# Kernel tuning notes

Hardware: AMD Instinct MI355X
Metric: run time of the kernel (lower is better)

Reference implementation:

```python
import jax, jax.numpy as jnp
import numpy as np

DIM = 64
OUT_DIM = 32
ALPHA = 16
BRANCH = 4
DEPTH = 7  # levels 0..DEPTH; level l has BRANCH**l nodes
SIZES = [BRANCH ** l for l in range(DEPTH + 1)]
OFFS = np.cumsum([0] + SIZES).tolist()  # OFFS[l] = start index of level l (BFS order)
N = OFFS[-1]  # 21845


def _build_children():
    # complete 4-ary tree in BFS order; leaves get 0 (never read)
    ch = np.zeros((N, BRANCH), dtype=np.int32)
    for l in range(DEPTH):
        off, size = OFFS[l], SIZES[l]
        base = OFFS[l + 1] + BRANCH * np.arange(size)
        ch[off:off + size] = base[:, None] + np.arange(BRANCH)[None, :]
    return jnp.asarray(ch)


def setup_inputs() -> dict:
    key = jax.random.key(0)
    k1, k2, k3, k4, k5 = jax.random.split(key, 5)
    sym = jax.random.randint(k1, (N,), 0, ALPHA, dtype=jnp.int32)
    children = _build_children()
    s = 1.0 / np.sqrt(DIM)
    W = jax.random.normal(k2, (ALPHA, DIM, DIM), dtype=jnp.float32) * s      # per-symbol Linear weight [out,in]
    b = jax.random.normal(k3, (ALPHA, DIM), dtype=jnp.float32) * s           # per-symbol Linear bias
    W_out = jax.random.normal(k4, (OUT_DIM, DIM), dtype=jnp.float32) * s
    b_out = jax.random.normal(k5, (OUT_DIM,), dtype=jnp.float32) * s
    return {"sym": sym, "children": children, "W": W, "b": b,
            "W_out": W_out, "b_out": b_out}


def _forward(W, b, W_out, b_out, sym, children):
    enc = jnp.zeros((N, DIM), dtype=W.dtype)
    # process levels bottom-up (children before parents) -- batches the
    # original node-by-node stack recursion by tree depth
    for l in range(DEPTH, -1, -1):
        off, size = OFFS[l], SIZES[l]
        syms = sym[off:off + size]                      # [size]
        if l == DEPTH:
            # leaves: layer applied to zero vector
            h = jnp.zeros((size, DIM), dtype=W.dtype)
        else:
            ch = children[off:off + size]               # [size, 4]
            h = enc[ch].mean(axis=1)                    # gather children encodings + mean
        Wn = W[syms]                                    # [size, dim, dim] symbol-routed weights
        bn = b[syms]                                    # [size, dim]
        e = jax.nn.sigmoid(jnp.einsum('nij,nj->ni', Wn, h) + bn)
        enc = enc.at[off:off + size].set(e)
    # root is node 0 in BFS order
    return enc[0] @ W_out.T + b_out                     # [OUT_DIM]


def reference(sym, children, W, b, W_out, b_out):
    return _forward(W, b, W_out, b_out, sym, children)
```

## Files before the change

### kernel.cpp

```cpp
#include <hip/hip_runtime.h>

#define DIM 64


__device__ __forceinline__ float sigmoidf_(float x) {
    return 1.0f / (1.0f + __expf(-x));
}

__device__ __forceinline__ float matvec_sig(const float* __restrict__ W,
                                            const float* __restrict__ B,
                                            int s, int lane,
                                            const float* h) {
    const float4* wrow = reinterpret_cast<const float4*>(W + (size_t)s * DIM * DIM + lane * DIM);
    const float4* h4   = reinterpret_cast<const float4*>(h);
    float acc = B[s * DIM + lane];
#pragma unroll
    for (int j = 0; j < DIM / 4; ++j) {
        float4 wv = wrow[j];
        float4 hv = h4[j];
        acc = fmaf(wv.x, hv.x, acc);
        acc = fmaf(wv.y, hv.y, acc);
        acc = fmaf(wv.z, hv.z, acc);
        acc = fmaf(wv.w, hv.w, acc);
    }
    return sigmoidf_(acc);
}

__global__ __launch_bounds__(1024) void k_lvl654(const int* __restrict__ sym,
                                                 const float* __restrict__ W,
                                                 const float* __restrict__ B,
                                                 float* __restrict__ enc4) {
    __shared__ __align__(16) float h6[16][DIM];
    __shared__ __align__(16) float e6[16][DIM];
    __shared__ __align__(16) float h5[4][DIM];
    __shared__ __align__(16) float e5[4][DIM];
    __shared__ __align__(16) float h4s[DIM];

    const int tid  = threadIdx.x;
    const int lane = tid & 63;
    const int w    = tid >> 6;
    const int b    = blockIdx.x;

    {
        int leaf0 = 5461 + b * 64 + w * 4;
        float acc = 0.0f;
#pragma unroll
        for (int c = 0; c < 4; ++c) {
            acc += sigmoidf_(B[sym[leaf0 + c] * DIM + lane]);
        }
        h6[w][lane] = 0.25f * acc;
    }
    __syncthreads();
    e6[w][lane] = matvec_sig(W, B, sym[1365 + b * 16 + w], lane, &h6[w][0]);
    __syncthreads();
    if (w < 4) {
        h5[w][lane] = 0.25f * (e6[4 * w + 0][lane] + e6[4 * w + 1][lane] +
                               e6[4 * w + 2][lane] + e6[4 * w + 3][lane]);
    }
    __syncthreads();
    if (w < 4) {
        e5[w][lane] = matvec_sig(W, B, sym[341 + b * 4 + w], lane, &h5[w][0]);
    }
    __syncthreads();
    if (w == 0) {
        h4s[lane] = 0.25f * (e5[0][lane] + e5[1][lane] + e5[2][lane] + e5[3][lane]);
    }
    __syncthreads();
    if (w == 0) {
        enc4[b * DIM + lane] = matvec_sig(W, B, sym[85 + b], lane, h4s);
    }
}

__global__ __launch_bounds__(256) void k_lvl32(const int* __restrict__ sym,
                                               const float* __restrict__ W,
                                               const float* __restrict__ B,
                                               const float* __restrict__ enc4,
                                               float* __restrict__ enc2) {
    __shared__ __align__(16) float h3[4][DIM];
    __shared__ __align__(16) float e3[4][DIM];
    __shared__ __align__(16) float hb[DIM];
    const int tid  = threadIdx.x;
    const int lane = tid & 63;
    const int w    = tid >> 6;
    const int b    = blockIdx.x;

    {
        int c0 = 16 * b + 4 * w;
        float acc = enc4[(c0 + 0) * DIM + lane] + enc4[(c0 + 1) * DIM + lane] +
                    enc4[(c0 + 2) * DIM + lane] + enc4[(c0 + 3) * DIM + lane];
        h3[w][lane] = 0.25f * acc;
    }
    __syncthreads();
    e3[w][lane] = matvec_sig(W, B, sym[21 + 4 * b + w], lane, &h3[w][0]);
    __syncthreads();
    if (w == 0) {
        hb[lane] = 0.25f * (e3[0][lane] + e3[1][lane] + e3[2][lane] + e3[3][lane]);
    }
    __syncthreads();
    if (w == 0) {
        enc2[b * DIM + lane] = matvec_sig(W, B, sym[5 + b], lane, hb);
    }
}

__global__ __launch_bounds__(256) void k_lvl10_out(const int* __restrict__ sym,
                                                   const float* __restrict__ W,
                                                   const float* __restrict__ B,
                                                   const float* __restrict__ Wout,
                                                   const float* __restrict__ bout,
                                                   const float* __restrict__ enc2,
                                                   float* __restrict__ out) {
    __shared__ __align__(16) float h1[4][DIM];
    __shared__ __align__(16) float e1[4][DIM];
    __shared__ __align__(16) float hb[DIM];
    __shared__ __align__(16) float e0[DIM];
    const int tid  = threadIdx.x;
    const int lane = tid & 63;
    const int w    = tid >> 6;

    {
        int c0 = 4 * w;
        float acc = enc2[(c0 + 0) * DIM + lane] + enc2[(c0 + 1) * DIM + lane] +
                    enc2[(c0 + 2) * DIM + lane] + enc2[(c0 + 3) * DIM + lane];
        h1[w][lane] = 0.25f * acc;
    }
    __syncthreads();
    e1[w][lane] = matvec_sig(W, B, sym[1 + w], lane, &h1[w][0]);
    __syncthreads();
    if (w == 0) {
        hb[lane] = 0.25f * (e1[0][lane] + e1[1][lane] + e1[2][lane] + e1[3][lane]);
    }
    __syncthreads();
    if (w == 0) {
        e0[lane] = matvec_sig(W, B, sym[0], lane, hb);
    }
    __syncthreads();
    if (tid < 32) {
        const float4* wrow = reinterpret_cast<const float4*>(Wout + tid * DIM);
        const float4* h4   = reinterpret_cast<const float4*>(e0);
        float acc = bout[tid];
#pragma unroll
        for (int j = 0; j < DIM / 4; ++j) {
            float4 wv = wrow[j];
            float4 hv = h4[j];
            acc = fmaf(wv.x, hv.x, acc);
            acc = fmaf(wv.y, hv.y, acc);
            acc = fmaf(wv.z, hv.z, acc);
            acc = fmaf(wv.w, hv.w, acc);
        }
        out[tid] = acc;
    }
}

extern "C" void kernel_launch(void* const* d_in, const int* in_sizes, int n_in,
                              void* d_out, int out_size, void* d_ws, size_t ws_size,
                              hipStream_t stream) {
    const int*   sym  = (const int*)d_in[0];
    const float* W    = (const float*)d_in[2];
    const float* B    = (const float*)d_in[3];
    const float* Wout = (const float*)d_in[4];
    const float* bout = (const float*)d_in[5];
    float* out  = (float*)d_out;
    float* enc4 = (float*)d_ws;
    float* enc2 = enc4 + 256 * DIM;

    k_lvl654<<<256, 1024, 0, stream>>>(sym, W, B, enc4);
    k_lvl32 <<<16,  256, 0, stream>>>(sym, W, B, enc4, enc2);
    k_lvl10_out<<<1, 256, 0, stream>>>(sym, W, B, Wout, bout, enc2, out);
}
```

Before: 84.52 us.

## Fuse three tree-level kernels into one using inter-block flag synchronization

Merges the level 6-4, level 3-2 and root/output kernels into a single launch. The last block of each group of 16 spins on global flags set by its siblings before computing levels 3-2, and block 255 waits on the 16 group flags to compute the root and the output projection. This removes two kernel launch boundaries and their drain/fill gaps. The risks are that spin-waiting assumes all blocks are co-resident, and that the flags are never reset between calls, so later calls may read stale flags instead of truly synchronizing.

```diff
diff --git a/kernel.cpp b/kernel.cpp
--- a/kernel.cpp
+++ b/kernel.cpp
@@ -1,6 +1,7 @@
 #include <hip/hip_runtime.h>
 
 #define DIM 64
+#define FLAG_MAGIC 0x13579BDFu
 
 
 __device__ __forceinline__ float sigmoidf_(float x) {
@@ -26,15 +27,22 @@
     return sigmoidf_(acc);
 }
 
-__global__ __launch_bounds__(1024) void k_lvl654(const int* __restrict__ sym,
-                                                 const float* __restrict__ W,
-                                                 const float* __restrict__ B,
-                                                 float* __restrict__ enc4) {
+__global__ __launch_bounds__(1024) void k_fused(const int* __restrict__ sym,
+                                                const float* __restrict__ W,
+                                                const float* __restrict__ B,
+                                                const float* __restrict__ Wout,
+                                                const float* __restrict__ bout,
+                                                float* __restrict__ enc4,
+                                                float* __restrict__ enc2,
+                                                unsigned* __restrict__ flag4,
+                                                unsigned* __restrict__ flag2,
+                                                float* __restrict__ out) {
     __shared__ __align__(16) float h6[16][DIM];
     __shared__ __align__(16) float e6[16][DIM];
     __shared__ __align__(16) float h5[4][DIM];
     __shared__ __align__(16) float e5[4][DIM];
-    __shared__ __align__(16) float h4s[DIM];
+    __shared__ __align__(16) float hx[DIM];
+    __shared__ __align__(16) float e0s[DIM];
 
     const int tid  = threadIdx.x;
     const int lane = tid & 63;
@@ -63,91 +71,96 @@
     }
     __syncthreads();
     if (w == 0) {
-        h4s[lane] = 0.25f * (e5[0][lane] + e5[1][lane] + e5[2][lane] + e5[3][lane]);
+        hx[lane] = 0.25f * (e5[0][lane] + e5[1][lane] + e5[2][lane] + e5[3][lane]);
     }
     __syncthreads();
     if (w == 0) {
-        enc4[b * DIM + lane] = matvec_sig(W, B, sym[85 + b], lane, h4s);
+        enc4[b * DIM + lane] = matvec_sig(W, B, sym[85 + b], lane, hx);
     }
-}
+    if (tid == 0) {
+        __threadfence();
+        __hip_atomic_store(&flag4[b], FLAG_MAGIC, __ATOMIC_RELAXED,
+                           __HIP_MEMORY_SCOPE_AGENT);
+    }
 
-__global__ __launch_bounds__(256) void k_lvl32(const int* __restrict__ sym,
-                                               const float* __restrict__ W,
-                                               const float* __restrict__ B,
-                                               const float* __restrict__ enc4,
-                                               float* __restrict__ enc2) {
-    __shared__ __align__(16) float h3[4][DIM];
-    __shared__ __align__(16) float e3[4][DIM];
-    __shared__ __align__(16) float hb[DIM];
-    const int tid  = threadIdx.x;
-    const int lane = tid & 63;
-    const int w    = tid >> 6;
-    const int b    = blockIdx.x;
+    const int g = b >> 4;
+    if ((b & 15) == 15) {
+        if (tid < 15) {
+            while (__hip_atomic_load(&flag4[g * 16 + tid], __ATOMIC_RELAXED,
+                                     __HIP_MEMORY_SCOPE_AGENT) != FLAG_MAGIC) {
+                __builtin_amdgcn_s_sleep(1);
+            }
+        }
+        __syncthreads();
+        __threadfence();
+        if (w < 4) {
+            int c0 = 16 * g + 4 * w;
+            float acc = enc4[(c0 + 0) * DIM + lane] + enc4[(c0 + 1) * DIM + lane] +
+                        enc4[(c0 + 2) * DIM + lane] + enc4[(c0 + 3) * DIM + lane];
+            h5[w][lane] = 0.25f * acc;
+        }
+        __syncthreads();
+        if (w < 4) {
+            e5[w][lane] = matvec_sig(W, B, sym[21 + 4 * g + w], lane, &h5[w][0]);
+        }
+        __syncthreads();
+        if (w == 0) {
+            hx[lane] = 0.25f * (e5[0][lane] + e5[1][lane] + e5[2][lane] + e5[3][lane]);
+        }
+        __syncthreads();
+        if (w == 0) {
+            enc2[g * DIM + lane] = matvec_sig(W, B, sym[5 + g], lane, hx);
+        }
+        if (tid == 0) {
+            __threadfence();
+            __hip_atomic_store(&flag2[g], FLAG_MAGIC, __ATOMIC_RELAXED,
+                               __HIP_MEMORY_SCOPE_AGENT);
+        }
+    }
 
-    {
-        int c0 = 16 * b + 4 * w;
-        float acc = enc4[(c0 + 0) * DIM + lane] + enc4[(c0 + 1) * DIM + lane] +
-                    enc4[(c0 + 2) * DIM + lane] + enc4[(c0 + 3) * DIM + lane];
-        h3[w][lane] = 0.25f * acc;
-    }
-    __syncthreads();
-    e3[w][lane] = matvec_sig(W, B, sym[21 + 4 * b + w], lane, &h3[w][0]);
-    __syncthreads();
-    if (w == 0) {
-        hb[lane] = 0.25f * (e3[0][lane] + e3[1][lane] + e3[2][lane] + e3[3][lane]);
-    }
-    __syncthreads();
-    if (w == 0) {
-        enc2[b * DIM + lane] = matvec_sig(W, B, sym[5 + b], lane, hb);
-    }
-}
-
-__global__ __launch_bounds__(256) void k_lvl10_out(const int* __restrict__ sym,
-                                                   const float* __restrict__ W,
-                                                   const float* __restrict__ B,
-                                                   const float* __restrict__ Wout,
-                                                   const float* __restrict__ bout,
-                                                   const float* __restrict__ enc2,
-                                                   float* __restrict__ out) {
-    __shared__ __align__(16) float h1[4][DIM];
-    __shared__ __align__(16) float e1[4][DIM];
-    __shared__ __align__(16) float hb[DIM];
-    __shared__ __align__(16) float e0[DIM];
-    const int tid  = threadIdx.x;
-    const int lane = tid & 63;
-    const int w    = tid >> 6;
-
-    {
-        int c0 = 4 * w;
-        float acc = enc2[(c0 + 0) * DIM + lane] + enc2[(c0 + 1) * DIM + lane] +
-                    enc2[(c0 + 2) * DIM + lane] + enc2[(c0 + 3) * DIM + lane];
-        h1[w][lane] = 0.25f * acc;
-    }
-    __syncthreads();
-    e1[w][lane] = matvec_sig(W, B, sym[1 + w], lane, &h1[w][0]);
-    __syncthreads();
-    if (w == 0) {
-        hb[lane] = 0.25f * (e1[0][lane] + e1[1][lane] + e1[2][lane] + e1[3][lane]);
-    }
-    __syncthreads();
-    if (w == 0) {
-        e0[lane] = matvec_sig(W, B, sym[0], lane, hb);
-    }
-    __syncthreads();
-    if (tid < 32) {
-        const float4* wrow = reinterpret_cast<const float4*>(Wout + tid * DIM);
-        const float4* h4   = reinterpret_cast<const float4*>(e0);
-        float acc = bout[tid];
+    if (b == 255) {
+        if (tid < 15) {
+            while (__hip_atomic_load(&flag2[tid], __ATOMIC_RELAXED,
+                                     __HIP_MEMORY_SCOPE_AGENT) != FLAG_MAGIC) {
+                __builtin_amdgcn_s_sleep(1);
+            }
+        }
+        __syncthreads();
+        __threadfence();
+        if (w < 4) {
+            int c0 = 4 * w;
+            float acc = enc2[(c0 + 0) * DIM + lane] + enc2[(c0 + 1) * DIM + lane] +
+                        enc2[(c0 + 2) * DIM + lane] + enc2[(c0 + 3) * DIM + lane];
+            h5[w][lane] = 0.25f * acc;
+        }
+        __syncthreads();
+        if (w < 4) {
+            e5[w][lane] = matvec_sig(W, B, sym[1 + w], lane, &h5[w][0]);
+        }
+        __syncthreads();
+        if (w == 0) {
+            hx[lane] = 0.25f * (e5[0][lane] + e5[1][lane] + e5[2][lane] + e5[3][lane]);
+        }
+        __syncthreads();
+        if (w == 0) {
+            e0s[lane] = matvec_sig(W, B, sym[0], lane, hx);
+        }
+        __syncthreads();
+        if (tid < 32) {
+            const float4* wrow = reinterpret_cast<const float4*>(Wout + tid * DIM);
+            const float4* h4   = reinterpret_cast<const float4*>(e0s);
+            float acc = bout[tid];
 #pragma unroll
-        for (int j = 0; j < DIM / 4; ++j) {
-            float4 wv = wrow[j];
-            float4 hv = h4[j];
-            acc = fmaf(wv.x, hv.x, acc);
-            acc = fmaf(wv.y, hv.y, acc);
-            acc = fmaf(wv.z, hv.z, acc);
-            acc = fmaf(wv.w, hv.w, acc);
+            for (int j = 0; j < DIM / 4; ++j) {
+                float4 wv = wrow[j];
+                float4 hv = h4[j];
+                acc = fmaf(wv.x, hv.x, acc);
+                acc = fmaf(wv.y, hv.y, acc);
+                acc = fmaf(wv.z, hv.z, acc);
+                acc = fmaf(wv.w, hv.w, acc);
+            }
+            out[tid] = acc;
         }
-        out[tid] = acc;
     }
 }
 
@@ -160,10 +173,12 @@
     const float* Wout = (const float*)d_in[4];
     const float* bout = (const float*)d_in[5];
     float* out  = (float*)d_out;
-    float* enc4 = (float*)d_ws;
-    float* enc2 = enc4 + 256 * DIM;
 
-    k_lvl654<<<256, 1024, 0, stream>>>(sym, W, B, enc4);
-    k_lvl32 <<<16,  256, 0, stream>>>(sym, W, B, enc4, enc2);
-    k_lvl10_out<<<1, 256, 0, stream>>>(sym, W, B, Wout, bout, enc2, out);
+    float*    enc4  = (float*)d_ws;
+    float*    enc2  = enc4 + 256 * DIM;
+    unsigned* flag4 = (unsigned*)(enc2 + 16 * DIM);
+    unsigned* flag2 = flag4 + 256;
+
+    k_fused<<<256, 1024, 0, stream>>>(sym, W, B, Wout, bout,
+                                      enc4, enc2, flag4, flag2, out);
 }
```

After: 118.6 us. 1.4x slower.

## Bucket level-6 nodes by symbol so each wave reuses one weight matrix

Applied to the files above, without the earlier changes.

In the first kernel, the 16 level-6 nodes of a block are grouped by their symbol using shared-memory atomic counters. Each wave then owns one symbol and applies that symbol's weight row to up to four nodes at once, so a weight row loaded from memory is reused across several matvecs. This is meant to cut redundant weight loads and improve instruction-level parallelism. The cost is load imbalance across waves, since symbol counts vary, plus an extra barrier and atomics.

```diff
diff --git a/kernel.cpp b/kernel.cpp
--- a/kernel.cpp
+++ b/kernel.cpp
@@ -35,12 +35,16 @@
     __shared__ __align__(16) float h5[4][DIM];
     __shared__ __align__(16) float e5[4][DIM];
     __shared__ __align__(16) float h4s[DIM];
+    __shared__ int cnt[16];
+    __shared__ int lists[16][16];
 
     const int tid  = threadIdx.x;
     const int lane = tid & 63;
     const int w    = tid >> 6;
     const int b    = blockIdx.x;
 
+    if (tid < 16) cnt[tid] = 0;
+
     {
         int leaf0 = 5461 + b * 64 + w * 4;
         float acc = 0.0f;
@@ -51,7 +55,50 @@
         h6[w][lane] = 0.25f * acc;
     }
     __syncthreads();
-    e6[w][lane] = matvec_sig(W, B, sym[1365 + b * 16 + w], lane, &h6[w][0]);
+
+    if (tid < 16) {
+        int s = sym[1365 + b * 16 + tid];
+        int k = atomicAdd(&cnt[s], 1);
+        lists[s][k] = tid;
+    }
+    __syncthreads();
+
+    {
+        const int c = cnt[w];
+        if (c > 0) {
+            const float4* wrow = reinterpret_cast<const float4*>(W + (size_t)w * DIM * DIM + lane * DIM);
+            const float bias = B[w * DIM + lane];
+            for (int base = 0; base < c; base += 4) {
+                const int m  = c - base;
+                const int i0 = lists[w][base];
+                const int i1 = lists[w][base + (m > 1 ? 1 : 0)];
+                const int i2 = lists[w][base + (m > 2 ? 2 : 0)];
+                const int i3 = lists[w][base + (m > 3 ? 3 : 0)];
+                const float4* p0 = reinterpret_cast<const float4*>(&h6[i0][0]);
+                const float4* p1 = reinterpret_cast<const float4*>(&h6[i1][0]);
+                const float4* p2 = reinterpret_cast<const float4*>(&h6[i2][0]);
+                const float4* p3 = reinterpret_cast<const float4*>(&h6[i3][0]);
+                float a0 = bias, a1 = bias, a2 = bias, a3 = bias;
+#pragma unroll
+                for (int j = 0; j < DIM / 4; ++j) {
+                    float4 wv = wrow[j];
+                    float4 v0 = p0[j], v1 = p1[j], v2 = p2[j], v3 = p3[j];
+                    a0 = fmaf(wv.x, v0.x, a0); a0 = fmaf(wv.y, v0.y, a0);
+                    a0 = fmaf(wv.z, v0.z, a0); a0 = fmaf(wv.w, v0.w, a0);
+                    a1 = fmaf(wv.x, v1.x, a1); a1 = fmaf(wv.y, v1.y, a1);
+                    a1 = fmaf(wv.z, v1.z, a1); a1 = fmaf(wv.w, v1.w, a1);
+                    a2 = fmaf(wv.x, v2.x, a2); a2 = fmaf(wv.y, v2.y, a2);
+                    a2 = fmaf(wv.z, v2.z, a2); a2 = fmaf(wv.w, v2.w, a2);
+                    a3 = fmaf(wv.x, v3.x, a3); a3 = fmaf(wv.y, v3.y, a3);
+                    a3 = fmaf(wv.z, v3.z, a3); a3 = fmaf(wv.w, v3.w, a3);
+                }
+                e6[i0][lane] = sigmoidf_(a0);
+                if (m > 1) e6[i1][lane] = sigmoidf_(a1);
+                if (m > 2) e6[i2][lane] = sigmoidf_(a2);
+                if (m > 3) e6[i3][lane] = sigmoidf_(a3);
+            }
+        }
+    }
     __syncthreads();
     if (w < 4) {
         h5[w][lane] = 0.25f * (e6[4 * w + 0][lane] + e6[4 * w + 1][lane] +
```

New measurement: 108.3 us. 1.28x slower.
